# Kernel tuning notes

Hardware: AMD Instinct MI355X
Metric: run time of the kernel (lower is better)

The kernel has to match this reference:

```python
import jax, jax.numpy as jnp
import numpy as np

N = 8192
E = 262144
C = 256          # in_channels
OUT = 256        # out_channels
H = 4            # num_heads
DH = C // H      # head dim


def setup_inputs() -> dict:
    key = jax.random.key(0)
    ks = jax.random.split(key, 12)
    stdv = 1.0 / np.sqrt(C)
    inp = {
        "x": jax.random.normal(ks[0], (N, C), dtype=jnp.float32),
        "adj": jax.random.randint(ks[1], (2, E), 0, N, dtype=jnp.int64),
        "weight_local": jax.random.uniform(ks[2], (C, C), jnp.float32, -stdv, stdv),
        # nn.MultiheadAttention packed projections
        "in_proj_w": jax.random.normal(ks[3], (3 * C, C), jnp.float32) * stdv,
        "in_proj_b": jnp.zeros((3 * C,), jnp.float32),
        "out_proj_w": jax.random.normal(ks[4], (C, C), jnp.float32) * stdv,
        "out_proj_b": jnp.zeros((C,), jnp.float32),
        "ln_g": jnp.ones((C,), jnp.float32),
        "ln_b": jnp.zeros((C,), jnp.float32),
        "alpha": jnp.zeros((), jnp.float32),
        "fc_w": jax.random.normal(ks[5], (OUT, C), jnp.float32) * stdv,
        "fc_b": jnp.zeros((OUT,), jnp.float32),
    }
    return inp


def _gcn_conv(x, edge_index):
    # out[col] += (1/sqrt(d[col]*d[row])) * x[row], d = in-degree by col
    row, col = edge_index[0], edge_index[1]
    n = x.shape[0]
    d = jax.ops.segment_sum(jnp.ones((edge_index.shape[1],), x.dtype), col, num_segments=n)
    val = jax.lax.rsqrt(d[col] * d[row])
    val = jnp.where(jnp.isfinite(val), val, 0.0)
    msg = x[row] * val[:, None]                      # [E, C] gather + scale
    return jax.ops.segment_sum(msg, col, num_segments=n)  # [N, C] scatter-add


def _mha(x, in_proj_w, in_proj_b, out_proj_w, out_proj_b):
    # single-batch self-attention over all N nodes
    qkv = x @ in_proj_w.T + in_proj_b                # [N, 3C]
    q, k, v = jnp.split(qkv, 3, axis=-1)
    def heads(t):
        return t.reshape(N, H, DH).transpose(1, 0, 2)  # [H, N, DH]
    q, k, v = heads(q), heads(k), heads(v)
    scores = jnp.einsum("hnd,hmd->hnm", q, k) / np.sqrt(DH)  # [H, N, N]
    attn = jax.nn.softmax(scores, axis=-1)
    out = jnp.einsum("hnm,hmd->hnd", attn, v)        # [H, N, DH]
    out = out.transpose(1, 0, 2).reshape(N, C)
    return out @ out_proj_w.T + out_proj_b


def _layernorm(x, g, b, eps=1e-5):
    mu = jnp.mean(x, axis=-1, keepdims=True)
    var = jnp.var(x, axis=-1, keepdims=True)
    return (x - mu) * jax.lax.rsqrt(var + eps) * g + b


def reference(x, adj, weight_local, in_proj_w, in_proj_b, out_proj_w, out_proj_b,
              ln_g, ln_b, alpha, fc_w, fc_b):
    hi = _gcn_conv(x, adj)
    local_embed = hi @ weight_local                   # [N, C]
    attn_out = _mha(x, in_proj_w, in_proj_b, out_proj_w, out_proj_b)
    global_embed = _layernorm(x + attn_out, ln_g, ln_b)
    w = jax.nn.sigmoid(alpha)
    combined = w * local_embed + (1.0 - w) * global_embed
    return combined @ fc_w.T + fc_b                   # [N, OUT]
```

## Files before the change

kernel.cpp:

```cpp
#include <hip/hip_runtime.h>
#include <hip/hip_bf16.h>
#include <math.h>

#define NN   8192
#define EE   262144
#define CC   256
#define HH   4

typedef __bf16 bf16;
typedef __bf16 bf16x8 __attribute__((ext_vector_type(8)));
typedef __bf16 bf16x4 __attribute__((ext_vector_type(4)));
typedef __bf16 bf16x2 __attribute__((ext_vector_type(2)));
typedef float  f32x4  __attribute__((ext_vector_type(4)));

static __device__ __forceinline__ bf16 f2bf(float f) { return (bf16)f; }

static __device__ __forceinline__ unsigned pk2(float a, float b) {
    __hip_bfloat162 h = __float22bfloat162_rn(float2{a, b});
    return *reinterpret_cast<unsigned*>(&h);
}

__global__ void prep_all(const float* __restrict__ x, bf16* __restrict__ xb,
                         const float* __restrict__ ipw, const float* __restrict__ opw,
                         const float* __restrict__ fcw, const float* __restrict__ wloc,
                         bf16* __restrict__ ipwb, bf16* __restrict__ opwb,
                         bf16* __restrict__ fcwb, bf16* __restrict__ wlTb,
                         const int* __restrict__ adj, int* __restrict__ ideg) {
    int b = blockIdx.x, t = threadIdx.x;
    if (b < 2048) {
        for (int i = b * 256 + t; i < NN * CC; i += 2048 * 256) xb[i] = f2bf(x[i]);
    } else if (b < 2816) { int i = (b - 2048) * 256 + t; ipwb[i] = f2bf(ipw[i]); }
    else if (b < 3072)   { int i = (b - 2816) * 256 + t; opwb[i] = f2bf(opw[i]); }
    else if (b < 3328)   { int i = (b - 3072) * 256 + t; fcwb[i] = f2bf(fcw[i]); }
    else if (b < 3584)   { int n = b - 3328;             wlTb[n * 256 + t] = f2bf(wloc[t * 256 + n]); }
    else {
        int e = (b - 3584) * 256 + t;
        if (e < EE) atomicAdd(&ideg[adj[EE + e]], 1);
    }
}

__global__ __launch_bounds__(256) void build_kv(const bf16* __restrict__ qkv,
                                                bf16* __restrict__ Kpk,
                                                bf16* __restrict__ Vpk) {
    __shared__ bf16 tl[64][72];
    const int bx = blockIdx.x;
    const int h  = blockIdx.y;
    const int tid = threadIdx.x;
    #pragma unroll
    for (int i = 0; i < 2; i++) {
        int u = tid + i * 256;
        int key = u >> 3, g = u & 7;
        *reinterpret_cast<bf16x8*>(&tl[key][g * 8]) =
            *reinterpret_cast<const bf16x8*>(qkv + (size_t)(bx * 64 + key) * 768 + 256 + h * 64 + g * 8);
    }
    __syncthreads();
    #pragma unroll
    for (int i = 0; i < 2; i++) {
        int ee = tid + i * 256;
        int l15 = ee & 15, quad = (ee >> 4) & 3, c = (ee >> 6) & 1, ktl = ee >> 7;
        int key_local = (ktl >> 1) * 32 + (l15 >> 2) * 8 + (ktl & 1) * 4 + (l15 & 3);
        bf16x8 v = *reinterpret_cast<const bf16x8*>(&tl[key_local][c * 32 + quad * 8]);
        *reinterpret_cast<bf16x8*>(Kpk + ((size_t)((h * 512 + bx * 4 + ktl) * 2 + c)) * 512
                                       + (quad * 16 + l15) * 8) = v;
    }
    __syncthreads();
    #pragma unroll
    for (int i = 0; i < 2; i++) {
        int u = tid + i * 256;
        int key = u >> 3, g = u & 7;
        *reinterpret_cast<bf16x8*>(&tl[key][g * 8]) =
            *reinterpret_cast<const bf16x8*>(qkv + (size_t)(bx * 64 + key) * 768 + 512 + h * 64 + g * 8);
    }
    __syncthreads();
    #pragma unroll
    for (int i = 0; i < 2; i++) {
        int ee = tid + i * 256;
        int l15 = ee & 15, quad = (ee >> 4) & 3, nt = (ee >> 6) & 3, kcl = ee >> 8;
        bf16x8 v;
        #pragma unroll
        for (int j = 0; j < 8; j++) v[j] = tl[kcl * 32 + quad * 8 + j][nt * 16 + l15];
        *reinterpret_cast<bf16x8*>(Vpk + ((size_t)((h * 256 + bx * 2 + kcl) * 4 + nt)) * 512
                                       + (quad * 16 + l15) * 8) = v;
    }
}

__global__ __launch_bounds__(256) void scan_offsets(const int* __restrict__ ideg,
        int* __restrict__ off, int* __restrict__ cursor, float* __restrict__ rs) {
    __shared__ int ps[256];
    const int tid = threadIdx.x;
    const int base = tid * 32;
    int loc[32];
    int s = 0;
    #pragma unroll
    for (int i = 0; i < 32; i++) { loc[i] = s; s += ideg[base + i]; }
    ps[tid] = s;
    __syncthreads();
    for (int d = 1; d < 256; d <<= 1) {
        int v = (tid >= d) ? ps[tid - d] : 0;
        __syncthreads();
        ps[tid] += v;
        __syncthreads();
    }
    int excl = ps[tid] - s;
    #pragma unroll
    for (int i = 0; i < 32; i++) {
        int o = excl + loc[i];
        off[base + i] = o;
        cursor[base + i] = o;
        int dg = ideg[base + i];
        rs[base + i] = dg > 0 ? rsqrtf((float)dg) : 0.f;
    }
    if (tid == 255) off[8192] = excl + s;
}

__global__ void fill_csr(const int* __restrict__ adj, int* __restrict__ cursor,
                         int* __restrict__ csr) {
    int e = blockIdx.x * 256 + threadIdx.x;
    if (e < EE) {
        int col = adj[EE + e];
        int pos = atomicAdd(&cursor[col], 1);
        csr[pos] = adj[e];
    }
}

__global__ __launch_bounds__(256) void gcn_gather3(const bf16* __restrict__ xb,
        const int* __restrict__ csr, const int* __restrict__ off,
        const float* __restrict__ rs, bf16* __restrict__ hib) {
    const int node = blockIdx.x * 2 + (threadIdx.x >> 7);
    const int j = threadIdx.x & 127;
    const int o = off[node];
    const int cnt = off[node + 1] - o;
    const float rsc = rs[node];
    const unsigned* xrow = (const unsigned*)xb;
    float a0 = 0.f, a1 = 0.f;
    int e = 0;
    for (; e + 8 <= cnt; e += 8) {
        int r[8];
        float v[8];
        unsigned u[8];
        #pragma unroll
        for (int i = 0; i < 8; i++) r[i] = csr[o + e + i];
        #pragma unroll
        for (int i = 0; i < 8; i++) v[i] = rsc * rs[r[i]];
        #pragma unroll
        for (int i = 0; i < 8; i++) u[i] = xrow[(size_t)r[i] * 128 + j];
        #pragma unroll
        for (int i = 0; i < 8; i++) {
            a0 += __uint_as_float(u[i] << 16) * v[i];
            a1 += __uint_as_float(u[i] & 0xffff0000u) * v[i];
        }
    }
    for (; e < cnt; e++) {
        int r0 = csr[o + e];
        float v0 = rsc * rs[r0];
        unsigned u0 = xrow[(size_t)r0 * 128 + j];
        a0 += __uint_as_float(u0 << 16) * v0;
        a1 += __uint_as_float(u0 & 0xffff0000u) * v0;
    }
    bf16x2 pk;
    pk[0] = f2bf(a0);
    pk[1] = f2bf(a1);
    ((bf16x2*)(hib + (size_t)node * CC))[j] = pk;
}

__global__ __launch_bounds__(256) void gemm_bt(
        const bf16* __restrict__ A, const bf16* __restrict__ W,
        const float* __restrict__ bias,
        float* __restrict__ outF, bf16* __restrict__ outB,
        int M, int N, int K) {
    const int tid  = threadIdx.x;
    const int wave = tid >> 6;
    const int lane = tid & 63;
    const int quad = lane >> 4;
    const int l15  = lane & 15;
    const int m0 = blockIdx.x * 128;
    const int n0 = blockIdx.y * 64;

    __shared__ bf16 Alds[128][72];
    __shared__ bf16 Wlds[64][72];

    f32x4 acc[2][4];
    #pragma unroll
    for (int mt = 0; mt < 2; mt++)
        #pragma unroll
        for (int nt = 0; nt < 4; nt++)
            acc[mt][nt] = (f32x4){0.f, 0.f, 0.f, 0.f};

    for (int k0 = 0; k0 < K; k0 += 64) {
        #pragma unroll
        for (int i = 0; i < 4; i++) {
            int u = tid + i * 256;
            int r = u >> 3;
            int cp = u & 7;
            *reinterpret_cast<bf16x8*>(&Alds[r][cp * 8]) =
                *reinterpret_cast<const bf16x8*>(A + (size_t)(m0 + r) * K + k0 + cp * 8);
        }
        #pragma unroll
        for (int i = 0; i < 2; i++) {
            int u = tid + i * 256;
            int r = u >> 3;
            int cp = u & 7;
            *reinterpret_cast<bf16x8*>(&Wlds[r][cp * 8]) =
                *reinterpret_cast<const bf16x8*>(W + (size_t)(n0 + r) * K + k0 + cp * 8);
        }
        __syncthreads();
        #pragma unroll
        for (int c = 0; c < 2; c++) {
            bf16x8 af[2], wf[4];
            #pragma unroll
            for (int mt = 0; mt < 2; mt++)
                af[mt] = *reinterpret_cast<const bf16x8*>(&Alds[wave * 32 + mt * 16 + l15][c * 32 + quad * 8]);
            #pragma unroll
            for (int nt = 0; nt < 4; nt++)
                wf[nt] = *reinterpret_cast<const bf16x8*>(&Wlds[nt * 16 + l15][c * 32 + quad * 8]);
            #pragma unroll
            for (int mt = 0; mt < 2; mt++)
                #pragma unroll
                for (int nt = 0; nt < 4; nt++)
                    acc[mt][nt] = __builtin_amdgcn_mfma_f32_16x16x32_bf16(af[mt], wf[nt], acc[mt][nt], 0, 0, 0);
        }
        __syncthreads();
    }
    #pragma unroll
    for (int mt = 0; mt < 2; mt++)
        #pragma unroll
        for (int nt = 0; nt < 4; nt++)
            #pragma unroll
            for (int r = 0; r < 4; r++) {
                int m = m0 + wave * 32 + mt * 16 + quad * 4 + r;
                int n = n0 + nt * 16 + l15;
                float v = acc[mt][nt][r];
                if (bias) v += bias[n];
                if (outF) outF[(size_t)m * N + n] = v;
                else      outB[(size_t)m * N + n] = f2bf(v);
            }
}

__global__ __launch_bounds__(512, 2) void flash_attn15(const bf16* __restrict__ qkv,
                                                       const bf16* __restrict__ Kpk,
                                                       const bf16* __restrict__ Vpk,
                                                       bf16* __restrict__ attnO) {
    const int tid  = threadIdx.x;
    const int w    = tid >> 6;
    const int g    = w >> 2;
    const int k4   = w & 3;
    const int lane = tid & 63;
    const int quad = lane >> 4;
    const int l15  = lane & 15;
    const int bx = blockIdx.x;
    const int h  = (bx & 7) >> 1;
    const int qb = (bx >> 3) * 2 + (bx & 1);
    const int qbase = qb * 128 + g * 64;

    __shared__ bf16 Osh[8][64][68];
    __shared__ float lsh[8][64];

    const float qs = 0.180336880f;
    bf16x8 qf[4][2];
    #pragma unroll
    for (int qt = 0; qt < 4; qt++)
        #pragma unroll
        for (int c = 0; c < 2; c++) {
            bf16x8 raw = *reinterpret_cast<const bf16x8*>(
                qkv + (size_t)(qbase + qt * 16 + l15) * 768 + h * 64 + c * 32 + quad * 8);
            #pragma unroll
            for (int j = 0; j < 8; j++) qf[qt][c][j] = f2bf((float)raw[j] * qs);
        }

    const bf16* Kb = Kpk + (size_t)h * 524288 + lane * 8;
    const bf16* Vb = Vpk + (size_t)h * 524288 + lane * 8;

    f32x4 oacc[4][4];
    #pragma unroll
    for (int qt = 0; qt < 4; qt++)
        #pragma unroll
        for (int nt = 0; nt < 4; nt++) oacc[qt][nt] = (f32x4){0.f, 0.f, 0.f, 0.f};
    f32x4 lacc[4];
    #pragma unroll
    for (int qt = 0; qt < 4; qt++) lacc[qt] = (f32x4){0.f, 0.f, 0.f, 0.f};
    bf16x8 onesf;
    #pragma unroll
    for (int j = 0; j < 8; j++) onesf[j] = f2bf(1.0f);
    const f32x4 z4 = (f32x4){0.f, 0.f, 0.f, 0.f};

    bf16x8 kfA[2][2], vfA[4], kfB[2][2], vfB[4];

    #define LOADKV(kc, kf, vf)                                                          \
        {                                                                               \
            _Pragma("unroll")                                                           \
            for (int s = 0; s < 2; s++)                                                 \
                _Pragma("unroll")                                                       \
                for (int c = 0; c < 2; c++)                                             \
                    kf[s][c] = *reinterpret_cast<const bf16x8*>(Kb + (kc) * 2048 + s * 1024 + c * 512); \
            _Pragma("unroll")                                                           \
            for (int nt = 0; nt < 4; nt++)                                              \
                vf[nt] = *reinterpret_cast<const bf16x8*>(Vb + (kc) * 2048 + nt * 512); \
        }

    #define COMPUTE(kf, vf)                                                             \
        {                                                                               \
            f32x4 sacc[2][4];                                                           \
            __builtin_amdgcn_s_setprio(1);                                              \
            _Pragma("unroll")                                                           \
            for (int s = 0; s < 2; s++)                                                 \
                _Pragma("unroll")                                                       \
                for (int qt = 0; qt < 4; qt++) {                                        \
                    sacc[s][qt] = __builtin_amdgcn_mfma_f32_16x16x32_bf16(kf[s][0], qf[qt][0], z4, 0, 0, 0); \
                    sacc[s][qt] = __builtin_amdgcn_mfma_f32_16x16x32_bf16(kf[s][1], qf[qt][1], sacc[s][qt], 0, 0, 0); \
                }                                                                       \
            __builtin_amdgcn_s_setprio(0);                                              \
            _Pragma("unroll")                                                           \
            for (int qt = 0; qt < 4; qt++) {                                            \
                float e0 = __builtin_amdgcn_exp2f(sacc[0][qt][0]);                      \
                float e1 = __builtin_amdgcn_exp2f(sacc[0][qt][1]);                      \
                float e2 = __builtin_amdgcn_exp2f(sacc[0][qt][2]);                      \
                float e3 = __builtin_amdgcn_exp2f(sacc[0][qt][3]);                      \
                float e4 = __builtin_amdgcn_exp2f(sacc[1][qt][0]);                      \
                float e5 = __builtin_amdgcn_exp2f(sacc[1][qt][1]);                      \
                float e6 = __builtin_amdgcn_exp2f(sacc[1][qt][2]);                      \
                float e7 = __builtin_amdgcn_exp2f(sacc[1][qt][3]);                      \
                union { bf16x8 v; unsigned u[4]; } pu;                                  \
                pu.u[0] = pk2(e0, e1);                                                  \
                pu.u[1] = pk2(e2, e3);                                                  \
                pu.u[2] = pk2(e4, e5);                                                  \
                pu.u[3] = pk2(e6, e7);                                                  \
                __builtin_amdgcn_s_setprio(1);                                          \
                _Pragma("unroll")                                                       \
                for (int nt = 0; nt < 4; nt++)                                          \
                    oacc[qt][nt] = __builtin_amdgcn_mfma_f32_16x16x32_bf16(pu.v, vf[nt], oacc[qt][nt], 0, 0, 0); \
                lacc[qt] = __builtin_amdgcn_mfma_f32_16x16x32_bf16(pu.v, onesf, lacc[qt], 0, 0, 0); \
                __builtin_amdgcn_s_setprio(0);                                          \
            }                                                                           \
        }

    LOADKV(k4, kfA, vfA);
    for (int it = 0; it < 64; it += 2) {
        const int kB = k4 + (it + 1) * 4;
        LOADKV(kB, kfB, vfB);
        COMPUTE(kfA, vfA);
        int kA2 = k4 + (it + 2) * 4;
        if (kA2 > 255) kA2 = k4;
        LOADKV(kA2, kfA, vfA);
        COMPUTE(kfB, vfB);
    }
    #undef LOADKV
    #undef COMPUTE

    #pragma unroll
    for (int qt = 0; qt < 4; qt++)
        #pragma unroll
        for (int nt = 0; nt < 4; nt++)
            #pragma unroll
            for (int r = 0; r < 4; r++)
                Osh[w][qt * 16 + quad * 4 + r][nt * 16 + l15] = f2bf(oacc[qt][nt][r]);
    if (l15 == 0) {
        #pragma unroll
        for (int qt = 0; qt < 4; qt++)
            #pragma unroll
            for (int r = 0; r < 4; r++)
                lsh[w][qt * 16 + quad * 4 + r] = lacc[qt][r];
    }
    __syncthreads();

    const int q7 = tid >> 2;
    const int gg = q7 >> 6;
    const int ql = q7 & 63;
    const int ds = (tid & 3) * 16;
    const int wb = gg * 4;
    float lsum = lsh[wb][ql] + lsh[wb + 1][ql] + lsh[wb + 2][ql] + lsh[wb + 3][ql];
    float linv = 1.f / lsum;
    float acc[16];
    #pragma unroll
    for (int i = 0; i < 16; i++) acc[i] = 0.f;
    #pragma unroll
    for (int v = 0; v < 4; v++) {
        bf16x8 o0 = *reinterpret_cast<const bf16x8*>(&Osh[wb + v][ql][ds]);
        bf16x8 o1 = *reinterpret_cast<const bf16x8*>(&Osh[wb + v][ql][ds + 8]);
        #pragma unroll
        for (int i = 0; i < 8; i++) { acc[i] += (float)o0[i]; acc[8 + i] += (float)o1[i]; }
    }
    bf16x8 ob0, ob1;
    #pragma unroll
    for (int i = 0; i < 8; i++) {
        ob0[i] = f2bf(acc[i] * linv);
        ob1[i] = f2bf(acc[8 + i] * linv);
    }
    bf16* dst = attnO + (size_t)(qb * 128 + q7) * CC + h * 64 + ds;
    *reinterpret_cast<bf16x8*>(dst) = ob0;
    *reinterpret_cast<bf16x8*>(dst + 8) = ob1;
}

__global__ __launch_bounds__(256) void gemm_ln_fc(
        const bf16* __restrict__ aOb, const bf16* __restrict__ opwb, const float* __restrict__ opb,
        const bf16* __restrict__ hib, const bf16* __restrict__ wlTb,
        const float* __restrict__ x, const float* __restrict__ lng, const float* __restrict__ lnb,
        const float* __restrict__ alp, const bf16* __restrict__ fcwb, const float* __restrict__ fcb,
        float* __restrict__ out) {
    const int tid = threadIdx.x;
    const int w = tid >> 6, lane = tid & 63, quad = lane >> 4, l15 = lane & 15;
    const int m0 = blockIdx.x * 16;
    const int n0w = w * 64;
    const f32x4 z4 = (f32x4){0.f, 0.f, 0.f, 0.f};

    __shared__ bf16 Ab[16][264];
    __shared__ float Xl[16][260];
    __shared__ float rsum[4][16], rsq[4][16];

    #pragma unroll
    for (int i = 0; i < 4; i++) {
        int u = tid + i * 256;
        int row = u >> 6, cp = (u & 63) * 4;
        *reinterpret_cast<f32x4*>(&Xl[row][cp]) =
            *reinterpret_cast<const f32x4*>(x + (size_t)(m0 + row) * CC + cp);
    }

    #pragma unroll
    for (int i = 0; i < 2; i++) {
        int u = tid + i * 256;
        int row = u >> 5, cp = (u & 31) * 8;
        *reinterpret_cast<bf16x8*>(&Ab[row][cp]) =
            *reinterpret_cast<const bf16x8*>(aOb + (size_t)(m0 + row) * CC + cp);
    }
    __syncthreads();
    f32x4 r0[4], r1[4], acc[4];
    #pragma unroll
    for (int nt = 0; nt < 4; nt++) acc[nt] = z4;
    for (int kc = 0; kc < 4; kc++)
        #pragma unroll
        for (int c = 0; c < 2; c++) {
            bf16x8 af = *reinterpret_cast<const bf16x8*>(&Ab[l15][kc * 64 + c * 32 + quad * 8]);
            #pragma unroll
            for (int nt = 0; nt < 4; nt++) {
                bf16x8 wf = *reinterpret_cast<const bf16x8*>(
                    opwb + (size_t)(n0w + nt * 16 + l15) * CC + kc * 64 + c * 32 + quad * 8);
                acc[nt] = __builtin_amdgcn_mfma_f32_16x16x32_bf16(af, wf, acc[nt], 0, 0, 0);
            }
        }
    #pragma unroll
    for (int nt = 0; nt < 4; nt++) r0[nt] = acc[nt];
    __syncthreads();

    #pragma unroll
    for (int i = 0; i < 2; i++) {
        int u = tid + i * 256;
        int row = u >> 5, cp = (u & 31) * 8;
        *reinterpret_cast<bf16x8*>(&Ab[row][cp]) =
            *reinterpret_cast<const bf16x8*>(hib + (size_t)(m0 + row) * CC + cp);
    }
    __syncthreads();
    #pragma unroll
    for (int nt = 0; nt < 4; nt++) acc[nt] = z4;
    for (int kc = 0; kc < 4; kc++)
        #pragma unroll
        for (int c = 0; c < 2; c++) {
            bf16x8 af = *reinterpret_cast<const bf16x8*>(&Ab[l15][kc * 64 + c * 32 + quad * 8]);
            #pragma unroll
            for (int nt = 0; nt < 4; nt++) {
                bf16x8 wf = *reinterpret_cast<const bf16x8*>(
                    wlTb + (size_t)(n0w + nt * 16 + l15) * CC + kc * 64 + c * 32 + quad * 8);
                acc[nt] = __builtin_amdgcn_mfma_f32_16x16x32_bf16(af, wf, acc[nt], 0, 0, 0);
            }
        }
    #pragma unroll
    for (int nt = 0; nt < 4; nt++) r1[nt] = acc[nt];
    __syncthreads();

    float v[4][4];
    #pragma unroll
    for (int nt = 0; nt < 4; nt++) {
        float bias0 = opb[n0w + nt * 16 + l15];
        #pragma unroll
        for (int r = 0; r < 4; r++)
            v[nt][r] = Xl[quad * 4 + r][n0w + nt * 16 + l15] + r0[nt][r] + bias0;
    }
    #pragma unroll
    for (int r = 0; r < 4; r++) {
        float s = v[0][r] + v[1][r] + v[2][r] + v[3][r];
        float s2 = v[0][r] * v[0][r] + v[1][r] * v[1][r] + v[2][r] * v[2][r] + v[3][r] * v[3][r];
        #pragma unroll
        for (int o = 1; o < 16; o <<= 1) { s += __shfl_xor(s, o); s2 += __shfl_xor(s2, o); }
        if (l15 == 0) { rsum[w][quad * 4 + r] = s; rsq[w][quad * 4 + r] = s2; }
    }
    __syncthreads();

    const float wgt = 1.f / (1.f + __expf(-alp[0]));
    float gv[4], bv[4], fb[4];
    #pragma unroll
    for (int nt = 0; nt < 4; nt++) {
        int n = n0w + nt * 16 + l15;
        gv[nt] = lng[n]; bv[nt] = lnb[n]; fb[nt] = fcb[n];
    }
    #pragma unroll
    for (int r = 0; r < 4; r++) {
        int row = quad * 4 + r;
        float S = rsum[0][row] + rsum[1][row] + rsum[2][row] + rsum[3][row];
        float S2 = rsq[0][row] + rsq[1][row] + rsq[2][row] + rsq[3][row];
        float mu = S * (1.f / CC);
        float var = S2 * (1.f / CC) - mu * mu;
        float rstd = rsqrtf(var + 1e-5f);
        #pragma unroll
        for (int nt = 0; nt < 4; nt++) {
            float ln = (v[nt][r] - mu) * rstd * gv[nt] + bv[nt];
            float cmb = wgt * r1[nt][r] + (1.f - wgt) * ln;
            Ab[row][n0w + nt * 16 + l15] = f2bf(cmb);
        }
    }
    __syncthreads();

    #pragma unroll
    for (int nt = 0; nt < 4; nt++) acc[nt] = z4;
    for (int kc = 0; kc < 4; kc++)
        #pragma unroll
        for (int c = 0; c < 2; c++) {
            bf16x8 af = *reinterpret_cast<const bf16x8*>(&Ab[l15][kc * 64 + c * 32 + quad * 8]);
            #pragma unroll
            for (int nt = 0; nt < 4; nt++) {
                bf16x8 wf = *reinterpret_cast<const bf16x8*>(
                    fcwb + (size_t)(n0w + nt * 16 + l15) * CC + kc * 64 + c * 32 + quad * 8);
                acc[nt] = __builtin_amdgcn_mfma_f32_16x16x32_bf16(af, wf, acc[nt], 0, 0, 0);
            }
        }
    #pragma unroll
    for (int nt = 0; nt < 4; nt++)
        #pragma unroll
        for (int r = 0; r < 4; r++)
            out[(size_t)(m0 + quad * 4 + r) * CC + n0w + nt * 16 + l15] = acc[nt][r] + fb[nt];
}

extern "C" void kernel_launch(void* const* d_in, const int* in_sizes, int n_in,
                              void* d_out, int out_size, void* d_ws, size_t ws_size,
                              hipStream_t stream) {
    (void)in_sizes; (void)n_in; (void)out_size; (void)ws_size;
    const float* x    = (const float*)d_in[0];
    const int*   adj  = (const int*)d_in[1];
    const float* wloc = (const float*)d_in[2];
    const float* ipw  = (const float*)d_in[3];
    const float* ipb  = (const float*)d_in[4];
    const float* opw  = (const float*)d_in[5];
    const float* opb  = (const float*)d_in[6];
    const float* lng  = (const float*)d_in[7];
    const float* lnb  = (const float*)d_in[8];
    const float* alp  = (const float*)d_in[9];
    const float* fcw  = (const float*)d_in[10];
    const float* fcb  = (const float*)d_in[11];
    float* out = (float*)d_out;

    char* p = (char*)d_ws;
    int*   ideg   = (int*)p;    p += (size_t)NN * 4;
    int*   off    = (int*)p;    p += (size_t)(NN + 1) * 4;
    int*   cursor = (int*)p;    p += (size_t)NN * 4;
    float* rs     = (float*)p;  p += (size_t)NN * 4;
    int*   csr    = (int*)p;    p += (size_t)EE * 4;
    bf16* xb    = (bf16*)p;   p += (size_t)NN * CC * 2;
    bf16* hib   = (bf16*)p;   p += (size_t)NN * CC * 2;
    bf16* ipwb  = (bf16*)p;   p += (size_t)768 * 256 * 2;
    bf16* wlTb  = (bf16*)p;   p += (size_t)256 * 256 * 2;
    bf16* opwb  = (bf16*)p;   p += (size_t)256 * 256 * 2;
    bf16* fcwb  = (bf16*)p;   p += (size_t)256 * 256 * 2;
    bf16* qkvb  = (bf16*)p;   p += (size_t)NN * 768 * 2;
    bf16* Kpk   = (bf16*)p;   p += (size_t)HH * 512 * 2 * 512 * 2;
    bf16* Vpk   = (bf16*)p;   p += (size_t)HH * 256 * 4 * 512 * 2;
    bf16* aOb   = (bf16*)p;   p += (size_t)NN * CC * 2;

    hipMemsetAsync(ideg, 0, (size_t)NN * 4, stream);

    prep_all<<<4608, 256, 0, stream>>>(x, xb, ipw, opw, fcw, wloc, ipwb, opwb, fcwb, wlTb, adj, ideg);
    scan_offsets<<<1, 256, 0, stream>>>(ideg, off, cursor, rs);
    fill_csr<<<EE / 256, 256, 0, stream>>>(adj, cursor, csr);
    gcn_gather3<<<NN / 2, 256, 0, stream>>>(xb, csr, off, rs, hib);

    gemm_bt<<<dim3(NN / 128, 768 / 64), 256, 0, stream>>>(xb, ipwb, ipb, nullptr, qkvb, NN, 768, 256);
    build_kv<<<dim3(NN / 64, HH), 256, 0, stream>>>(qkvb, Kpk, Vpk);
    flash_attn15<<<256, 512, 0, stream>>>(qkvb, Kpk, Vpk, aOb);
    gemm_ln_fc<<<NN / 16, 256, 0, stream>>>(aOb, opwb, opb, hib, wlTb, x, lng, lnb, alp, fcwb, fcb, out);
}
```

Before: 252.1 us.

## Software-pipeline QK^T one chunk ahead of softmax/PV in flash attention

Restructures the attention inner loop so the QK^T MFMAs for the next key chunk are issued before the exp/PV work of the current chunk, with K and V loads split and staggered. The goal is to overlap the transcendental exp and packing work with matrix-core work and hide load latency. It keeps two score accumulator sets live, which raises register pressure under the 512x2 launch bound and may cause spills.

```diff
diff --git a/kernel.cpp b/kernel.cpp
--- a/kernel.cpp
+++ b/kernel.cpp
@@ -236,7 +236,7 @@
             }
 }
 
-__global__ __launch_bounds__(512, 2) void flash_attn15(const bf16* __restrict__ qkv,
+__global__ __launch_bounds__(512, 2) void flash_attn16(const bf16* __restrict__ qkv,
                                                        const bf16* __restrict__ Kpk,
                                                        const bf16* __restrict__ Vpk,
                                                        bf16* __restrict__ attnO) {
@@ -284,41 +284,46 @@
     const f32x4 z4 = (f32x4){0.f, 0.f, 0.f, 0.f};
 
     bf16x8 kfA[2][2], vfA[4], kfB[2][2], vfB[4];
-
-    #define LOADKV(kc, kf, vf)                                                          \
+    f32x4 sA[2][4], sB[2][4];
+
+    #define LOADK(kc, kf)                                                               \
         {                                                                               \
             _Pragma("unroll")                                                           \
             for (int s = 0; s < 2; s++)                                                 \
                 _Pragma("unroll")                                                       \
                 for (int c = 0; c < 2; c++)                                             \
                     kf[s][c] = *reinterpret_cast<const bf16x8*>(Kb + (kc) * 2048 + s * 1024 + c * 512); \
+        }
+    #define LOADV(kc, vf)                                                               \
+        {                                                                               \
             _Pragma("unroll")                                                           \
             for (int nt = 0; nt < 4; nt++)                                              \
                 vf[nt] = *reinterpret_cast<const bf16x8*>(Vb + (kc) * 2048 + nt * 512); \
         }
-
-    #define COMPUTE(kf, vf)                                                             \
+    #define QKT(kf, sc)                                                                 \
         {                                                                               \
-            f32x4 sacc[2][4];                                                           \
             __builtin_amdgcn_s_setprio(1);                                              \
             _Pragma("unroll")                                                           \
             for (int s = 0; s < 2; s++)                                                 \
                 _Pragma("unroll")                                                       \
                 for (int qt = 0; qt < 4; qt++) {                                        \
-                    sacc[s][qt] = __builtin_amdgcn_mfma_f32_16x16x32_bf16(kf[s][0], qf[qt][0], z4, 0, 0, 0); \
-                    sacc[s][qt] = __builtin_amdgcn_mfma_f32_16x16x32_bf16(kf[s][1], qf[qt][1], sacc[s][qt], 0, 0, 0); \
+                    sc[s][qt] = __builtin_amdgcn_mfma_f32_16x16x32_bf16(kf[s][0], qf[qt][0], z4, 0, 0, 0); \
+                    sc[s][qt] = __builtin_amdgcn_mfma_f32_16x16x32_bf16(kf[s][1], qf[qt][1], sc[s][qt], 0, 0, 0); \
                 }                                                                       \
             __builtin_amdgcn_s_setprio(0);                                              \
+        }
+    #define SOFTPV(sc, vf)                                                              \
+        {                                                                               \
             _Pragma("unroll")                                                           \
             for (int qt = 0; qt < 4; qt++) {                                            \
-                float e0 = __builtin_amdgcn_exp2f(sacc[0][qt][0]);                      \
-                float e1 = __builtin_amdgcn_exp2f(sacc[0][qt][1]);                      \
-                float e2 = __builtin_amdgcn_exp2f(sacc[0][qt][2]);                      \
-                float e3 = __builtin_amdgcn_exp2f(sacc[0][qt][3]);                      \
-                float e4 = __builtin_amdgcn_exp2f(sacc[1][qt][0]);                      \
-                float e5 = __builtin_amdgcn_exp2f(sacc[1][qt][1]);                      \
-                float e6 = __builtin_amdgcn_exp2f(sacc[1][qt][2]);                      \
-                float e7 = __builtin_amdgcn_exp2f(sacc[1][qt][3]);                      \
+                float e0 = __builtin_amdgcn_exp2f(sc[0][qt][0]);                        \
+                float e1 = __builtin_amdgcn_exp2f(sc[0][qt][1]);                        \
+                float e2 = __builtin_amdgcn_exp2f(sc[0][qt][2]);                        \
+                float e3 = __builtin_amdgcn_exp2f(sc[0][qt][3]);                        \
+                float e4 = __builtin_amdgcn_exp2f(sc[1][qt][0]);                        \
+                float e5 = __builtin_amdgcn_exp2f(sc[1][qt][1]);                        \
+                float e6 = __builtin_amdgcn_exp2f(sc[1][qt][2]);                        \
+                float e7 = __builtin_amdgcn_exp2f(sc[1][qt][3]);                        \
                 union { bf16x8 v; unsigned u[4]; } pu;                                  \
                 pu.u[0] = pk2(e0, e1);                                                  \
                 pu.u[1] = pk2(e2, e3);                                                  \
@@ -333,18 +338,25 @@
             }                                                                           \
         }
 
-    LOADKV(k4, kfA, vfA);
+    LOADK(k4, kfA); LOADV(k4, vfA);
+    LOADK(k4 + 4, kfB); LOADV(k4 + 4, vfB);
+    QKT(kfA, sA);
     for (int it = 0; it < 64; it += 2) {
-        const int kB = k4 + (it + 1) * 4;
-        LOADKV(kB, kfB, vfB);
-        COMPUTE(kfA, vfA);
-        int kA2 = k4 + (it + 2) * 4;
-        if (kA2 > 255) kA2 = k4;
-        LOADKV(kA2, kfA, vfA);
-        COMPUTE(kfB, vfB);
-    }
-    #undef LOADKV
-    #undef COMPUTE
+        QKT(kfB, sB);
+        int c2 = k4 + (it + 2) * 4; if (it + 2 > 63) c2 = k4;
+        LOADK(c2, kfA);
+        SOFTPV(sA, vfA);
+        LOADV(c2, vfA);
+        QKT(kfA, sA);
+        int c3 = k4 + (it + 3) * 4; if (it + 3 > 63) c3 = k4;
+        LOADK(c3, kfB);
+        SOFTPV(sB, vfB);
+        LOADV(c3, vfB);
+    }
+    #undef LOADK
+    #undef LOADV
+    #undef QKT
+    #undef SOFTPV
 
     #pragma unroll
     for (int qt = 0; qt < 4; qt++)
@@ -571,6 +583,6 @@
 
     gemm_bt<<<dim3(NN / 128, 768 / 64), 256, 0, stream>>>(xb, ipwb, ipb, nullptr, qkvb, NN, 768, 256);
     build_kv<<<dim3(NN / 64, HH), 256, 0, stream>>>(qkvb, Kpk, Vpk);
-    flash_attn15<<<256, 512, 0, stream>>>(qkvb, Kpk, Vpk, aOb);
+    flash_attn16<<<256, 512, 0, stream>>>(qkvb, Kpk, Vpk, aOb);
     gemm_ln_fc<<<NN / 16, 256, 0, stream>>>(aOb, opwb, opb, hib, wlTb, x, lng, lnb, alp, fcwb, fcb, out);
 }
```

Measured after the change: 253.2 us. No clear change (+0.5%).
